# Optimization experiments

Hardware: AMD Instinct MI355X
Metric: run time of the kernel (lower is better)

## Reference

```python
import jax, jax.numpy as jnp
import numpy as np

B, S, D = 1, 4096, 1024
H, DK, DV = 16, 64, 64


def setup_inputs() -> dict:
    key = jax.random.key(0)
    ks = jax.random.split(key, 12)
    s = 0.02
    return {
        "queries": jax.random.normal(ks[0], (B, S, D), jnp.float32),
        "keys": jax.random.normal(ks[1], (B, S, D), jnp.float32),
        "values": jax.random.normal(ks[2], (B, S, D), jnp.float32),
        "Wq": jax.random.normal(ks[3], (H * DK, D), jnp.float32) * s,
        "bq": jnp.zeros((H * DK,), jnp.float32),
        "Wk": jax.random.normal(ks[4], (H * DK, D), jnp.float32) * s,
        "bk": jnp.zeros((H * DK,), jnp.float32),
        "Wv": jax.random.normal(ks[5], (H * DV, D), jnp.float32) * s,
        "bv": jnp.zeros((H * DV,), jnp.float32),
        "Wo": jax.random.normal(ks[6], (D, H * DV), jnp.float32) * s,
        "bo": jnp.zeros((D,), jnp.float32),
    }


def reference(queries, keys, values, Wq, bq, Wk, bk, Wv, bv, Wo, bo):
    b, sq, _ = queries.shape
    sk = keys.shape[1]
    # projections -> [b, h, s, d]
    q = (queries @ Wq.T + bq).reshape(b, sq, H, DK).transpose(0, 2, 1, 3)
    k = (keys @ Wk.T + bk).reshape(b, sk, H, DK).transpose(0, 2, 1, 3)
    v = (values @ Wv.T + bv).reshape(b, sk, H, DV).transpose(0, 2, 1, 3)
    scores = jnp.einsum('bhqd,bhkd->bhqk', q, k) / jnp.sqrt(jnp.float32(DK))
    # causal mask (is_causal=True): disallow j > i
    causal = jnp.triu(jnp.ones((sq, sk), bool), k=1)
    scores = jnp.where(causal, jnp.float32(-jnp.inf), scores)
    attn = jax.nn.softmax(scores, axis=-1)
    out = jnp.einsum('bhqk,bhkd->bhqd', attn, v)
    out = out.transpose(0, 2, 1, 3).reshape(b, sq, H * DV)
    return out @ Wo.T + bo
```

## Files before the change

kernel.cpp:

```cpp
#include <hip/hip_runtime.h>

#define DEVI __device__ __forceinline__

typedef __attribute__((ext_vector_type(8))) short bf16x8;
typedef __attribute__((ext_vector_type(4))) float f32x4;

#define SQL 4096
#define DM 1024
#define NH 16
#define HD 64
#define S64 (SQL * HD)

DEVI unsigned short f2bf(float f) {
  unsigned int u = __float_as_uint(f);
  unsigned int r = (u + 0x7FFFu + ((u >> 16) & 1u)) >> 16;
  return (unsigned short)r;
}

DEVI void gl16(const void* g, void* l) {
  __builtin_amdgcn_global_load_lds((const __attribute__((address_space(1))) void*)g,
                                   (__attribute__((address_space(3))) void*)l, 16, 0, 0);
}

DEVI float rmax16(float v) {
  v = fmaxf(v, __shfl_xor(v, 1));
  v = fmaxf(v, __shfl_xor(v, 2));
  v = fmaxf(v, __shfl_xor(v, 4));
  v = fmaxf(v, __shfl_xor(v, 8));
  return v;
}
DEVI float rsum16(float v) {
  v += __shfl_xor(v, 1);
  v += __shfl_xor(v, 2);
  v += __shfl_xor(v, 4);
  v += __shfl_xor(v, 8);
  return v;
}

DEVI f32x4 mfma16(bf16x8 a, bf16x8 b, f32x4 c) {
  return __builtin_amdgcn_mfma_f32_16x16x32_bf16(a, b, c, 0, 0, 0);
}

__global__ void cvt_all(const float* __restrict__ q, const float* __restrict__ k,
                        const float* __restrict__ v, const float* __restrict__ Wq,
                        const float* __restrict__ Wk, const float* __restrict__ Wv,
                        const float* __restrict__ Wo, unsigned short* __restrict__ o) {
  const size_t SD = (size_t)SQL * DM, DD = (size_t)DM * DM;
  size_t i = ((size_t)blockIdx.x * 256 + threadIdx.x) * 4;
  const float* src;
  size_t base;
  if (i < SD) { src = q; base = 0; }
  else if (i < 2 * SD) { src = k; base = SD; }
  else if (i < 3 * SD) { src = v; base = 2 * SD; }
  else if (i < 3 * SD + DD) { src = Wq; base = 3 * SD; }
  else if (i < 3 * SD + 2 * DD) { src = Wk; base = 3 * SD + DD; }
  else if (i < 3 * SD + 3 * DD) { src = Wv; base = 3 * SD + 2 * DD; }
  else { src = Wo; base = 3 * SD + 3 * DD; }
  float4 vv = *reinterpret_cast<const float4*>(src + (i - base));
  ushort4 ov;
  ov.x = f2bf(vv.x); ov.y = f2bf(vv.y); ov.z = f2bf(vv.z); ov.w = f2bf(vv.w);
  *reinterpret_cast<ushort4*>(o + i) = ov;
}

__global__ __launch_bounds__(256) void gemm_qkv(
    const unsigned short* __restrict__ xq, const unsigned short* __restrict__ xk,
    const unsigned short* __restrict__ xv, const unsigned short* __restrict__ wq,
    const unsigned short* __restrict__ wk, const unsigned short* __restrict__ wv,
    const float* __restrict__ bq, const float* __restrict__ bk, const float* __restrict__ bv,
    unsigned short* __restrict__ Qh, unsigned short* __restrict__ Kh,
    unsigned short* __restrict__ VT) {
  __shared__ __align__(16) unsigned short lA[128 * 64];
  __shared__ __align__(16) unsigned short lB[128 * 64];
  const int z = blockIdx.z;
  const unsigned short* A = (z == 0) ? xq : (z == 1) ? xk : xv;
  const unsigned short* B = (z == 0) ? wq : (z == 1) ? wk : wv;
  const float* bias = (z == 0) ? bq : (z == 1) ? bk : bv;

  const int t = threadIdx.x;
  const int wid = t >> 6, lane = t & 63, lr = lane & 15, lg = lane >> 4;
  const int wm = wid >> 1, wn = wid & 1;
  const int m0 = blockIdx.y * 128, n0 = blockIdx.x * 128;
  const int K = DM, N = DM;

  f32x4 acc[4][4] = {};

  for (int kb = 0; kb < K; kb += 64) {
    __syncthreads();
#pragma unroll
    for (int i = 0; i < 4; i++) {
      const int u = i * 256 + t;
      const int row = u >> 3;
      const int ke = (u & 7) * 8;
      unsigned short* la = lA + (size_t)(i * 256 + wid * 64) * 8;
      unsigned short* lb = lB + (size_t)(i * 256 + wid * 64) * 8;
      gl16(A + (size_t)(m0 + row) * K + kb + ke, la);
      gl16(B + (size_t)(n0 + row) * K + kb + ke, lb);
    }
    __syncthreads();
#pragma unroll
    for (int kk = 0; kk < 2; kk++) {
      bf16x8 af[4], bfr[4];
#pragma unroll
      for (int m = 0; m < 4; m++)
        af[m] = *reinterpret_cast<const bf16x8*>(&lA[(wm * 64 + m * 16 + lr) * 64 + kk * 32 + lg * 8]);
#pragma unroll
      for (int n = 0; n < 4; n++)
        bfr[n] = *reinterpret_cast<const bf16x8*>(&lB[(wn * 64 + n * 16 + lr) * 64 + kk * 32 + lg * 8]);
#pragma unroll
      for (int m = 0; m < 4; m++)
#pragma unroll
        for (int n = 0; n < 4; n++)
          acc[m][n] = mfma16(af[m], bfr[n], acc[m][n]);
    }
  }

  unsigned short* dstQK = (z == 0) ? Qh : Kh;
#pragma unroll
  for (int m = 0; m < 4; m++)
#pragma unroll
    for (int n = 0; n < 4; n++) {
      const int col = n0 + wn * 64 + n * 16 + lr;
      const int h = col >> 6, d = col & 63;
      const int row0 = m0 + wm * 64 + m * 16 + lg * 4;
      const float bsv = bias[col];
      if (z < 2) {
#pragma unroll
        for (int r = 0; r < 4; r++)
          dstQK[(size_t)h * S64 + (size_t)(row0 + r) * HD + d] = f2bf(acc[m][n][r] + bsv);
      } else {
        ushort4 ov;
        ov.x = f2bf(acc[m][n][0] + bsv);
        ov.y = f2bf(acc[m][n][1] + bsv);
        ov.z = f2bf(acc[m][n][2] + bsv);
        ov.w = f2bf(acc[m][n][3] + bsv);
        *reinterpret_cast<ushort4*>(&VT[(size_t)h * S64 + (size_t)d * SQL + row0]) = ov;
      }
    }
}

__global__ __launch_bounds__(256) void gemm_out(
    const unsigned short* __restrict__ A, const unsigned short* __restrict__ B,
    const float* __restrict__ bias, float* __restrict__ C) {
  __shared__ __align__(16) unsigned short lA[128 * 64];
  __shared__ __align__(16) unsigned short lB[128 * 64];
  const int t = threadIdx.x;
  const int wid = t >> 6, lane = t & 63, lr = lane & 15, lg = lane >> 4;
  const int wm = wid >> 1, wn = wid & 1;
  const int m0 = blockIdx.y * 128, n0 = blockIdx.x * 128;
  const int K = DM, N = DM;

  f32x4 acc[4][4] = {};

  for (int kb = 0; kb < K; kb += 64) {
    __syncthreads();
#pragma unroll
    for (int i = 0; i < 4; i++) {
      const int u = i * 256 + t;
      const int row = u >> 3;
      const int ke = (u & 7) * 8;
      unsigned short* la = lA + (size_t)(i * 256 + wid * 64) * 8;
      unsigned short* lb = lB + (size_t)(i * 256 + wid * 64) * 8;
      gl16(A + (size_t)(m0 + row) * K + kb + ke, la);
      gl16(B + (size_t)(n0 + row) * K + kb + ke, lb);
    }
    __syncthreads();
#pragma unroll
    for (int kk = 0; kk < 2; kk++) {
      bf16x8 af[4], bfr[4];
#pragma unroll
      for (int m = 0; m < 4; m++)
        af[m] = *reinterpret_cast<const bf16x8*>(&lA[(wm * 64 + m * 16 + lr) * 64 + kk * 32 + lg * 8]);
#pragma unroll
      for (int n = 0; n < 4; n++)
        bfr[n] = *reinterpret_cast<const bf16x8*>(&lB[(wn * 64 + n * 16 + lr) * 64 + kk * 32 + lg * 8]);
#pragma unroll
      for (int m = 0; m < 4; m++)
#pragma unroll
        for (int n = 0; n < 4; n++)
          acc[m][n] = mfma16(af[m], bfr[n], acc[m][n]);
    }
  }

#pragma unroll
  for (int m = 0; m < 4; m++)
#pragma unroll
    for (int n = 0; n < 4; n++)
#pragma unroll
      for (int r = 0; r < 4; r++) {
        const int row = m0 + wm * 64 + m * 16 + lg * 4 + r;
        const int col = n0 + wn * 64 + n * 16 + lr;
        C[(size_t)row * N + col] = acc[m][n][r] + bias[col];
      }
}

__global__ __launch_bounds__(256) void attn_fwd(
    const unsigned short* __restrict__ Qh, const unsigned short* __restrict__ Kh,
    const unsigned short* __restrict__ VT, unsigned short* __restrict__ Ob) {
  const int bid = blockIdx.x;
  const int h = bid & 15;
  const int i6 = bid >> 4;
  const int jj = i6 & 15, bb = i6 >> 4;
  const int qt = (bb & 1) ? (bb * 16 + 15 - jj) : (bb * 16 + jj);
  const int t = threadIdx.x;
  const int wid = t >> 6, lane = t & 63, lr = lane & 15, lg = lane >> 4;
  const int q0 = qt * 64;

  __shared__ __align__(16) unsigned short Kt[2][4096];
  __shared__ __align__(16) unsigned short Vt[2][4096];
  __shared__ __align__(16) unsigned short Pl[4][1024];

  const unsigned short* Kp = Kh + (size_t)h * S64;
  const unsigned short* Vp = VT + (size_t)h * S64;

  bf16x8 qf[2];
  {
    const unsigned short* qp = Qh + (size_t)h * S64 + (size_t)(q0 + wid * 16 + lr) * HD + lg * 8;
    qf[0] = *reinterpret_cast<const bf16x8*>(qp);
    qf[1] = *reinterpret_cast<const bf16x8*>(qp + 32);
  }

  f32x4 accO[4] = {};
  float mrow[4] = {-INFINITY, -INFINITY, -INFINITY, -INFINITY};
  float lrow[4] = {0.f, 0.f, 0.f, 0.f};

  const int xsw = (lr & 7) << 4;
  unsigned short* pw = &Pl[wid][0];

  const int ntile = qt + 1;

#pragma unroll
  for (int ro = 0; ro < 2; ro++) {
    const int u = ro * 256 + t;
    const int row = u >> 3, slot = (u & 7) ^ (row & 7);
    gl16(Kp + (size_t)row * HD + slot * 8, &Kt[0][(ro * 256 + wid * 64) * 8]);
    gl16(Vp + (size_t)row * SQL + slot * 8, &Vt[0][(ro * 256 + wid * 64) * 8]);
  }

  int cur = 0;
  for (int tk = 0; tk < ntile; tk++) {
    const int kv0 = tk * 64;
    __syncthreads();

    if (tk + 1 < ntile) {
      const int nkv = kv0 + 64;
      unsigned short* kd = Kt[cur ^ 1];
      unsigned short* vd = Vt[cur ^ 1];
#pragma unroll
      for (int ro = 0; ro < 2; ro++) {
        const int u = ro * 256 + t;
        const int row = u >> 3, slot = (u & 7) ^ (row & 7);
        gl16(Kp + (size_t)(nkv + row) * HD + slot * 8, kd + (ro * 256 + wid * 64) * 8);
        gl16(Vp + (size_t)row * SQL + nkv + slot * 8, vd + (ro * 256 + wid * 64) * 8);
      }
    }

    const char* kt = (const char*)Kt[cur];
    const char* vt = (const char*)Vt[cur];

    f32x4 s[4];
#pragma unroll
    for (int ks = 0; ks < 4; ks++) {
      const char* rb = kt + (ks * 16 + lr) * 128;
      bf16x8 kf0 = *reinterpret_cast<const bf16x8*>(rb + ((lg * 16) ^ xsw));
      bf16x8 kf1 = *reinterpret_cast<const bf16x8*>(rb + ((64 + lg * 16) ^ xsw));
      f32x4 a = {};
      a = mfma16(qf[0], kf0, a);
      a = mfma16(qf[1], kf1, a);
      s[ks] = a;
    }

    if (tk == qt) {
#pragma unroll
      for (int ks = 0; ks < 4; ks++) {
        const int kg = kv0 + ks * 16 + lr;
#pragma unroll
        for (int r = 0; r < 4; r++) {
          const int qg = q0 + wid * 16 + lg * 4 + r;
          s[ks][r] = (kg <= qg) ? s[ks][r] * 0.125f : -INFINITY;
        }
      }
    } else {
#pragma unroll
      for (int ks = 0; ks < 4; ks++)
#pragma unroll
        for (int r = 0; r < 4; r++) s[ks][r] *= 0.125f;
    }

    float a4[4];
#pragma unroll
    for (int r = 0; r < 4; r++) {
      float tm = fmaxf(fmaxf(s[0][r], s[1][r]), fmaxf(s[2][r], s[3][r]));
      tm = rmax16(tm);
      const float mn = fmaxf(mrow[r], tm);
      const float al = __expf(mrow[r] - mn);
      mrow[r] = mn;
      float rs = 0.f;
#pragma unroll
      for (int ks = 0; ks < 4; ks++) {
        float pv = __expf(s[ks][r] - mn);
        s[ks][r] = pv;
        rs += pv;
      }
      rs = rsum16(rs);
      lrow[r] = lrow[r] * al + rs;
      a4[r] = al;
    }
#pragma unroll
    for (int dv = 0; dv < 4; dv++)
#pragma unroll
      for (int r = 0; r < 4; r++) accO[dv][r] *= a4[r];

#pragma unroll
    for (int ks = 0; ks < 4; ks++)
#pragma unroll
      for (int r = 0; r < 4; r++) {
        const int q = lg * 4 + r, kv = ks * 16 + lr;
        *(unsigned short*)((char*)pw + q * 128 + ((kv * 2) ^ ((q & 7) << 4))) = f2bf(s[ks][r]);
      }

    const char* pr = (const char*)pw + lr * 128;
    bf16x8 pa0 = *reinterpret_cast<const bf16x8*>(pr + ((lg * 16) ^ xsw));
    bf16x8 pa1 = *reinterpret_cast<const bf16x8*>(pr + ((64 + lg * 16) ^ xsw));

#pragma unroll
    for (int dv = 0; dv < 4; dv++) {
      const char* rb = vt + (dv * 16 + lr) * 128;
      bf16x8 vb0 = *reinterpret_cast<const bf16x8*>(rb + ((lg * 16) ^ xsw));
      bf16x8 vb1 = *reinterpret_cast<const bf16x8*>(rb + ((64 + lg * 16) ^ xsw));
      accO[dv] = mfma16(pa0, vb0, accO[dv]);
      accO[dv] = mfma16(pa1, vb1, accO[dv]);
    }
    cur ^= 1;
  }

#pragma unroll
  for (int dv = 0; dv < 4; dv++)
#pragma unroll
    for (int r = 0; r < 4; r++) {
      const int row = q0 + wid * 16 + lg * 4 + r;
      const int col = h * HD + dv * 16 + lr;
      Ob[(size_t)row * DM + col] = f2bf(accO[dv][r] / lrow[r]);
    }
}

extern "C" void kernel_launch(void* const* d_in, const int* in_sizes, int n_in,
                              void* d_out, int out_size, void* d_ws, size_t ws_size,
                              hipStream_t stream) {
  const float* queries = (const float*)d_in[0];
  const float* keys    = (const float*)d_in[1];
  const float* values  = (const float*)d_in[2];
  const float* Wq = (const float*)d_in[3];
  const float* bq = (const float*)d_in[4];
  const float* Wk = (const float*)d_in[5];
  const float* bk = (const float*)d_in[6];
  const float* Wv = (const float*)d_in[7];
  const float* bv = (const float*)d_in[8];
  const float* Wo = (const float*)d_in[9];
  const float* bo = (const float*)d_in[10];
  float* out = (float*)d_out;

  const size_t SD = (size_t)SQL * DM;
  const size_t DD = (size_t)DM * DM;

  unsigned short* p = (unsigned short*)d_ws;
  unsigned short* xq = p; p += SD;
  unsigned short* xk = p; p += SD;
  unsigned short* xv = p; p += SD;
  unsigned short* wq = p; p += DD;
  unsigned short* wk = p; p += DD;
  unsigned short* wv = p; p += DD;
  unsigned short* wo = p; p += DD;
  unsigned short* Qh = p; p += SD;
  unsigned short* Kh = p; p += SD;
  unsigned short* VTg = p; p += SD;
  unsigned short* Ob = xq;

  const int ncvt = (int)((3 * SD + 4 * DD) / 1024);
  cvt_all<<<ncvt, 256, 0, stream>>>(queries, keys, values, Wq, Wk, Wv, Wo, xq);

  gemm_qkv<<<dim3(DM / 128, SQL / 128, 3), 256, 0, stream>>>(
      xq, xk, xv, wq, wk, wv, bq, bk, bv, Qh, Kh, VTg);

  attn_fwd<<<1024, 256, 0, stream>>>(Qh, Kh, VTg, Ob);

  gemm_out<<<dim3(DM / 128, SQL / 128), 256, 0, stream>>>(Ob, wo, bo, out);
}
```

Baseline: 331.9 us.

## Rewrite attention with 32x32 MFMA, S-transposed layout and lazy rescaling

The attention kernel moves from 16x16x32 MFMA with 4 waves to 32x32x16 MFMA with 2 waves. Each wave owns 32 query rows, computing S^T so that a lane holds one query's scores. This removes the cross-lane shuffle reductions and the LDS round-trip for P, which is now built in registers with packed bf16 converts and a lane-32 swap. The softmax scale and log2(e) are folded into Q in the QKV epilogue so exp2f can be used, and the running-max rescale is skipped unless the max grows by more than 8. The V-transpose epilogue is staged through LDS for vectorized 16-byte stores. The trade-off is fewer threads per block and higher register pressure.

```diff
diff --git a/kernel.cpp b/kernel.cpp
--- a/kernel.cpp
+++ b/kernel.cpp
@@ -4,6 +4,7 @@
 
 typedef __attribute__((ext_vector_type(8))) short bf16x8;
 typedef __attribute__((ext_vector_type(4))) float f32x4;
+typedef __attribute__((ext_vector_type(16))) float f32x16;
 
 #define SQL 4096
 #define DM 1024
@@ -22,23 +23,17 @@
                                    (__attribute__((address_space(3))) void*)l, 16, 0, 0);
 }
 
-DEVI float rmax16(float v) {
-  v = fmaxf(v, __shfl_xor(v, 1));
-  v = fmaxf(v, __shfl_xor(v, 2));
-  v = fmaxf(v, __shfl_xor(v, 4));
-  v = fmaxf(v, __shfl_xor(v, 8));
-  return v;
-}
-DEVI float rsum16(float v) {
-  v += __shfl_xor(v, 1);
-  v += __shfl_xor(v, 2);
-  v += __shfl_xor(v, 4);
-  v += __shfl_xor(v, 8);
-  return v;
-}
-
 DEVI f32x4 mfma16(bf16x8 a, bf16x8 b, f32x4 c) {
   return __builtin_amdgcn_mfma_f32_16x16x32_bf16(a, b, c, 0, 0, 0);
+}
+DEVI f32x16 mfma32(bf16x8 a, bf16x8 b, f32x16 c) {
+  return __builtin_amdgcn_mfma_f32_32x32x16_bf16(a, b, c, 0, 0, 0);
+}
+
+DEVI unsigned cvtpk(float lo, float hi) {
+  unsigned r;
+  asm("v_cvt_pk_bf16_f32 %0, %1, %2" : "=v"(r) : "v"(lo), "v"(hi));
+  return r;
 }
 
 __global__ void cvt_all(const float* __restrict__ q, const float* __restrict__ k,
@@ -69,8 +64,9 @@
     const float* __restrict__ bq, const float* __restrict__ bk, const float* __restrict__ bv,
     unsigned short* __restrict__ Qh, unsigned short* __restrict__ Kh,
     unsigned short* __restrict__ VT) {
-  __shared__ __align__(16) unsigned short lA[128 * 64];
-  __shared__ __align__(16) unsigned short lB[128 * 64];
+  __shared__ __align__(16) unsigned short smem[17408];
+  unsigned short* lA = smem;
+  unsigned short* lB = smem + 8192;
   const int z = blockIdx.z;
   const unsigned short* A = (z == 0) ? xq : (z == 1) ? xk : xv;
   const unsigned short* B = (z == 0) ? wq : (z == 1) ? wk : wv;
@@ -80,7 +76,7 @@
   const int wid = t >> 6, lane = t & 63, lr = lane & 15, lg = lane >> 4;
   const int wm = wid >> 1, wn = wid & 1;
   const int m0 = blockIdx.y * 128, n0 = blockIdx.x * 128;
-  const int K = DM, N = DM;
+  const int K = DM;
 
   f32x4 acc[4][4] = {};
 
@@ -114,28 +110,46 @@
     }
   }
 
-  unsigned short* dstQK = (z == 0) ? Qh : Kh;
-#pragma unroll
-  for (int m = 0; m < 4; m++)
-#pragma unroll
-    for (int n = 0; n < 4; n++) {
-      const int col = n0 + wn * 64 + n * 16 + lr;
-      const int h = col >> 6, d = col & 63;
-      const int row0 = m0 + wm * 64 + m * 16 + lg * 4;
-      const float bsv = bias[col];
-      if (z < 2) {
+  if (z < 2) {
+    const float sc = (z == 0) ? 0.18033688f : 1.0f;
+    unsigned short* dst = (z == 0) ? Qh : Kh;
+#pragma unroll
+    for (int m = 0; m < 4; m++)
+#pragma unroll
+      for (int n = 0; n < 4; n++) {
+        const int col = n0 + wn * 64 + n * 16 + lr;
+        const int hh = col >> 6, d = col & 63;
+        const int row0 = m0 + wm * 64 + m * 16 + lg * 4;
+        const float bsv = bias[col];
 #pragma unroll
         for (int r = 0; r < 4; r++)
-          dstQK[(size_t)h * S64 + (size_t)(row0 + r) * HD + d] = f2bf(acc[m][n][r] + bsv);
-      } else {
-        ushort4 ov;
-        ov.x = f2bf(acc[m][n][0] + bsv);
-        ov.y = f2bf(acc[m][n][1] + bsv);
-        ov.z = f2bf(acc[m][n][2] + bsv);
-        ov.w = f2bf(acc[m][n][3] + bsv);
-        *reinterpret_cast<ushort4*>(&VT[(size_t)h * S64 + (size_t)d * SQL + row0]) = ov;
-      }
-    }
+          dst[(size_t)hh * S64 + (size_t)(row0 + r) * HD + d] = f2bf((acc[m][n][r] + bsv) * sc);
+      }
+  } else {
+    __syncthreads();
+#pragma unroll
+    for (int m = 0; m < 4; m++)
+#pragma unroll
+      for (int n = 0; n < 4; n++) {
+        const int col = n0 + wn * 64 + n * 16 + lr;
+        const int dt = wn * 64 + n * 16 + lr;
+        const float bsv = bias[col];
+#pragma unroll
+        for (int r = 0; r < 4; r++) {
+          const int st = wm * 64 + m * 16 + lg * 4 + r;
+          smem[dt * 136 + st] = f2bf(acc[m][n][r] + bsv);
+        }
+      }
+    __syncthreads();
+#pragma unroll
+    for (int it = 0; it < 8; it++) {
+      const int u = it * 256 + t;
+      const int d = u >> 4, sc8 = (u & 15) * 8;
+      const int col = n0 + d, hh = col >> 6, dd = col & 63;
+      *reinterpret_cast<uint4*>(VT + (size_t)hh * S64 + (size_t)dd * SQL + m0 + sc8) =
+          *reinterpret_cast<const uint4*>(&smem[d * 136 + sc8]);
+    }
+  }
 }
 
 __global__ __launch_bounds__(256) void gemm_out(
@@ -193,7 +207,7 @@
       }
 }
 
-__global__ __launch_bounds__(256) void attn_fwd(
+__global__ __launch_bounds__(128) void attn_fwd(
     const unsigned short* __restrict__ Qh, const unsigned short* __restrict__ Kh,
     const unsigned short* __restrict__ VT, unsigned short* __restrict__ Ob) {
   const int bid = blockIdx.x;
@@ -202,38 +216,37 @@
   const int jj = i6 & 15, bb = i6 >> 4;
   const int qt = (bb & 1) ? (bb * 16 + 15 - jj) : (bb * 16 + jj);
   const int t = threadIdx.x;
-  const int wid = t >> 6, lane = t & 63, lr = lane & 15, lg = lane >> 4;
+  const int wid = t >> 6, lane = t & 63;
+  const int ql = lane & 31, hi = lane >> 5;
   const int q0 = qt * 64;
+  const int q_g = q0 + wid * 32 + ql;
 
   __shared__ __align__(16) unsigned short Kt[2][4096];
   __shared__ __align__(16) unsigned short Vt[2][4096];
-  __shared__ __align__(16) unsigned short Pl[4][1024];
 
   const unsigned short* Kp = Kh + (size_t)h * S64;
   const unsigned short* Vp = VT + (size_t)h * S64;
 
-  bf16x8 qf[2];
+  bf16x8 qf[4];
   {
-    const unsigned short* qp = Qh + (size_t)h * S64 + (size_t)(q0 + wid * 16 + lr) * HD + lg * 8;
-    qf[0] = *reinterpret_cast<const bf16x8*>(qp);
-    qf[1] = *reinterpret_cast<const bf16x8*>(qp + 32);
-  }
-
-  f32x4 accO[4] = {};
-  float mrow[4] = {-INFINITY, -INFINITY, -INFINITY, -INFINITY};
-  float lrow[4] = {0.f, 0.f, 0.f, 0.f};
-
-  const int xsw = (lr & 7) << 4;
-  unsigned short* pw = &Pl[wid][0];
-
+    const unsigned short* qp = Qh + (size_t)h * S64 + (size_t)q_g * HD + hi * 8;
+#pragma unroll
+    for (int c = 0; c < 4; c++)
+      qf[c] = *reinterpret_cast<const bf16x8*>(qp + c * 16);
+  }
+
+  f32x16 accO[2] = {};
+  float m = -INFINITY, l = 0.f;
+
+  const int xm = (ql & 7) << 4;
   const int ntile = qt + 1;
 
 #pragma unroll
-  for (int ro = 0; ro < 2; ro++) {
-    const int u = ro * 256 + t;
+  for (int ro = 0; ro < 4; ro++) {
+    const int u = ro * 128 + t;
     const int row = u >> 3, slot = (u & 7) ^ (row & 7);
-    gl16(Kp + (size_t)row * HD + slot * 8, &Kt[0][(ro * 256 + wid * 64) * 8]);
-    gl16(Vp + (size_t)row * SQL + slot * 8, &Vt[0][(ro * 256 + wid * 64) * 8]);
+    gl16(Kp + (size_t)row * HD + slot * 8, &Kt[0][(ro * 128 + wid * 64) * 8]);
+    gl16(Vp + (size_t)row * SQL + slot * 8, &Vt[0][(ro * 128 + wid * 64) * 8]);
   }
 
   int cur = 0;
@@ -243,103 +256,118 @@
 
     if (tk + 1 < ntile) {
       const int nkv = kv0 + 64;
-      unsigned short* kd = Kt[cur ^ 1];
-      unsigned short* vd = Vt[cur ^ 1];
-#pragma unroll
-      for (int ro = 0; ro < 2; ro++) {
-        const int u = ro * 256 + t;
+      unsigned short* kdb = Kt[cur ^ 1];
+      unsigned short* vdb = Vt[cur ^ 1];
+#pragma unroll
+      for (int ro = 0; ro < 4; ro++) {
+        const int u = ro * 128 + t;
         const int row = u >> 3, slot = (u & 7) ^ (row & 7);
-        gl16(Kp + (size_t)(nkv + row) * HD + slot * 8, kd + (ro * 256 + wid * 64) * 8);
-        gl16(Vp + (size_t)row * SQL + nkv + slot * 8, vd + (ro * 256 + wid * 64) * 8);
+        gl16(Kp + (size_t)(nkv + row) * HD + slot * 8, kdb + (ro * 128 + wid * 64) * 8);
+        gl16(Vp + (size_t)row * SQL + nkv + slot * 8, vdb + (ro * 128 + wid * 64) * 8);
       }
     }
 
     const char* kt = (const char*)Kt[cur];
     const char* vt = (const char*)Vt[cur];
 
-    f32x4 s[4];
-#pragma unroll
-    for (int ks = 0; ks < 4; ks++) {
-      const char* rb = kt + (ks * 16 + lr) * 128;
-      bf16x8 kf0 = *reinterpret_cast<const bf16x8*>(rb + ((lg * 16) ^ xsw));
-      bf16x8 kf1 = *reinterpret_cast<const bf16x8*>(rb + ((64 + lg * 16) ^ xsw));
-      f32x4 a = {};
-      a = mfma16(qf[0], kf0, a);
-      a = mfma16(qf[1], kf1, a);
-      s[ks] = a;
-    }
+    f32x16 sA[2];
+    __builtin_amdgcn_s_setprio(1);
+#pragma unroll
+    for (int kc = 0; kc < 2; kc++) {
+      const char* rb = kt + (32 * kc + ql) * 128;
+      f32x16 a = {};
+#pragma unroll
+      for (int c = 0; c < 4; c++) {
+        bf16x8 kf = *reinterpret_cast<const bf16x8*>(rb + ((c * 32 + hi * 16) ^ xm));
+        a = mfma32(kf, qf[c], a);
+      }
+      sA[kc] = a;
+    }
+    __builtin_amdgcn_s_setprio(0);
 
     if (tk == qt) {
 #pragma unroll
-      for (int ks = 0; ks < 4; ks++) {
-        const int kg = kv0 + ks * 16 + lr;
-#pragma unroll
-        for (int r = 0; r < 4; r++) {
-          const int qg = q0 + wid * 16 + lg * 4 + r;
-          s[ks][r] = (kg <= qg) ? s[ks][r] * 0.125f : -INFINITY;
+      for (int kc = 0; kc < 2; kc++)
+#pragma unroll
+        for (int r = 0; r < 16; r++) {
+          const int kv_g = kv0 + 32 * kc + (r & 3) + 8 * (r >> 2) + 4 * hi;
+          if (kv_g > q_g) sA[kc][r] = -INFINITY;
         }
-      }
-    } else {
-#pragma unroll
-      for (int ks = 0; ks < 4; ks++)
-#pragma unroll
-        for (int r = 0; r < 4; r++) s[ks][r] *= 0.125f;
-    }
-
-    float a4[4];
-#pragma unroll
-    for (int r = 0; r < 4; r++) {
-      float tm = fmaxf(fmaxf(s[0][r], s[1][r]), fmaxf(s[2][r], s[3][r]));
-      tm = rmax16(tm);
-      const float mn = fmaxf(mrow[r], tm);
-      const float al = __expf(mrow[r] - mn);
-      mrow[r] = mn;
-      float rs = 0.f;
-#pragma unroll
-      for (int ks = 0; ks < 4; ks++) {
-        float pv = __expf(s[ks][r] - mn);
-        s[ks][r] = pv;
-        rs += pv;
-      }
-      rs = rsum16(rs);
-      lrow[r] = lrow[r] * al + rs;
-      a4[r] = al;
-    }
-#pragma unroll
-    for (int dv = 0; dv < 4; dv++)
-#pragma unroll
-      for (int r = 0; r < 4; r++) accO[dv][r] *= a4[r];
-
-#pragma unroll
-    for (int ks = 0; ks < 4; ks++)
-#pragma unroll
-      for (int r = 0; r < 4; r++) {
-        const int q = lg * 4 + r, kv = ks * 16 + lr;
-        *(unsigned short*)((char*)pw + q * 128 + ((kv * 2) ^ ((q & 7) << 4))) = f2bf(s[ks][r]);
-      }
-
-    const char* pr = (const char*)pw + lr * 128;
-    bf16x8 pa0 = *reinterpret_cast<const bf16x8*>(pr + ((lg * 16) ^ xsw));
-    bf16x8 pa1 = *reinterpret_cast<const bf16x8*>(pr + ((64 + lg * 16) ^ xsw));
-
-#pragma unroll
-    for (int dv = 0; dv < 4; dv++) {
-      const char* rb = vt + (dv * 16 + lr) * 128;
-      bf16x8 vb0 = *reinterpret_cast<const bf16x8*>(rb + ((lg * 16) ^ xsw));
-      bf16x8 vb1 = *reinterpret_cast<const bf16x8*>(rb + ((64 + lg * 16) ^ xsw));
-      accO[dv] = mfma16(pa0, vb0, accO[dv]);
-      accO[dv] = mfma16(pa1, vb1, accO[dv]);
-    }
+    }
+
+    float pm = sA[0][0];
+#pragma unroll
+    for (int r = 1; r < 16; r++) pm = fmaxf(pm, sA[0][r]);
+#pragma unroll
+    for (int r = 0; r < 16; r++) pm = fmaxf(pm, sA[1][r]);
+    pm = fmaxf(pm, __shfl_xor(pm, 32));
+    if (!__all(pm - m <= 8.f)) {
+      const float mn = fmaxf(m, pm);
+      const float al = exp2f(m - mn);
+      m = mn;
+      l *= al;
+#pragma unroll
+      for (int dc = 0; dc < 2; dc++)
+#pragma unroll
+        for (int r = 0; r < 16; r++) accO[dc][r] *= al;
+    }
+    float sum = 0.f;
+#pragma unroll
+    for (int kc = 0; kc < 2; kc++)
+#pragma unroll
+      for (int r = 0; r < 16; r++) {
+        const float e = exp2f(sA[kc][r] - m);
+        sA[kc][r] = e;
+        sum += e;
+      }
+    sum += __shfl_xor(sum, 32);
+    l += sum;
+
+    bf16x8 pf[4];
+#pragma unroll
+    for (int ck = 0; ck < 4; ck++) {
+      const int kc = ck >> 1, rb0 = (ck & 1) * 8;
+      unsigned lo0 = cvtpk(sA[kc][rb0 + 0], sA[kc][rb0 + 1]);
+      unsigned lo1 = cvtpk(sA[kc][rb0 + 2], sA[kc][rb0 + 3]);
+      unsigned h0  = cvtpk(sA[kc][rb0 + 4], sA[kc][rb0 + 5]);
+      unsigned h1  = cvtpk(sA[kc][rb0 + 6], sA[kc][rb0 + 7]);
+      unsigned xl0 = (unsigned)__shfl_xor((int)lo0, 32);
+      unsigned xl1 = (unsigned)__shfl_xor((int)lo1, 32);
+      unsigned xh0 = (unsigned)__shfl_xor((int)h0, 32);
+      unsigned xh1 = (unsigned)__shfl_xor((int)h1, 32);
+      unsigned* pw = (unsigned*)&pf[ck];
+      pw[0] = hi ? xh0 : lo0;
+      pw[1] = hi ? xh1 : lo1;
+      pw[2] = hi ? h0 : xl0;
+      pw[3] = hi ? h1 : xl1;
+    }
+
+    __builtin_amdgcn_s_setprio(1);
+#pragma unroll
+    for (int dc = 0; dc < 2; dc++) {
+      const char* rb = vt + (32 * dc + ql) * 128;
+#pragma unroll
+      for (int ck = 0; ck < 4; ck++) {
+        bf16x8 vf = *reinterpret_cast<const bf16x8*>(rb + ((ck * 32 + hi * 16) ^ xm));
+        accO[dc] = mfma32(vf, pf[ck], accO[dc]);
+      }
+    }
+    __builtin_amdgcn_s_setprio(0);
     cur ^= 1;
   }
 
-#pragma unroll
-  for (int dv = 0; dv < 4; dv++)
-#pragma unroll
-    for (int r = 0; r < 4; r++) {
-      const int row = q0 + wid * 16 + lg * 4 + r;
-      const int col = h * HD + dv * 16 + lr;
-      Ob[(size_t)row * DM + col] = f2bf(accO[dv][r] / lrow[r]);
+  const float inv = 1.f / l;
+  unsigned short* ob = Ob + (size_t)q_g * DM + h * HD;
+#pragma unroll
+  for (int dc = 0; dc < 2; dc++)
+#pragma unroll
+    for (int tq = 0; tq < 4; tq++) {
+      ushort4 o;
+      o.x = f2bf(accO[dc][tq * 4 + 0] * inv);
+      o.y = f2bf(accO[dc][tq * 4 + 1] * inv);
+      o.z = f2bf(accO[dc][tq * 4 + 2] * inv);
+      o.w = f2bf(accO[dc][tq * 4 + 3] * inv);
+      *reinterpret_cast<ushort4*>(ob + dc * 32 + tq * 8 + hi * 4) = o;
     }
 }
 
@@ -381,7 +409,7 @@
   gemm_qkv<<<dim3(DM / 128, SQL / 128, 3), 256, 0, stream>>>(
       xq, xk, xv, wq, wk, wv, bq, bk, bv, Qh, Kh, VTg);
 
-  attn_fwd<<<1024, 256, 0, stream>>>(Qh, Kh, VTg, Ob);
+  attn_fwd<<<1024, 128, 0, stream>>>(Qh, Kh, VTg, Ob);
 
   gemm_out<<<dim3(DM / 128, SQL / 128), 256, 0, stream>>>(Ob, wo, bo, out);
 }
```

New measurement: 322.5 us. 2.8% less time.
